# Kernel optimization log

Hardware: AMD Instinct MI355X
Metric: run time of the kernel (lower is better)

## Reference

```python
import jax, jax.numpy as jnp
import numpy as np

NELEMS = 1_000_000
FEAT = 128
NSEG = 1024


def setup_inputs() -> dict:
    key = jax.random.key(0)
    k1, k2 = jax.random.split(key)
    memory = jax.random.normal(k1, (NELEMS, FEAT), dtype=jnp.float32)
    m_batch = jnp.sort(jax.random.randint(k2, (NELEMS,), 0, NSEG, dtype=jnp.int64))
    return {"memory": memory, "m_batch": m_batch, "num_segments": NSEG}


def reference(memory, m_batch, num_segments):
    # torch.sparse.sum over dim=1 of a [nbatches, nelems, F] COO tensor built from
    # (batch, arange) indices == per-batch segment sum of memory rows.
    return jax.ops.segment_sum(memory, m_batch, num_segments=num_segments)
```

## Files before the change

kernel.cpp:

```cpp
#include <hip/hip_runtime.h>


#define FEAT 128
#define F4 (FEAT / 4)
#define ROWLANES 16
#define THREADS (F4 * ROWLANES)

typedef float f32x4 __attribute__((ext_vector_type(4)));

__global__ __launch_bounds__(THREADS, 8) void segsum_fused(
        const f32x4* __restrict__ mem,
        const int* __restrict__ seg,
        f32x4* __restrict__ out,
        int nelems) {
    const int b    = blockIdx.x;
    const int lane = threadIdx.x & (F4 - 1);
    const int rl   = threadIdx.x >> 5;

    __shared__ int sb[2];

    if (threadIdx.x < 64) {
        const int half = threadIdx.x >> 5;
        const int j    = threadIdx.x & 31;
        const int t    = b + half;

        int lo = 0, len = nelems;
        #pragma unroll
        for (int round = 0; round < 4; ++round) {
            int pos = lo + (int)(((long long)j * len) >> 5);
            int v = seg[pos];
            unsigned long long m = __ballot(v < t);
            unsigned mh = half ? (unsigned)(m >> 32) : (unsigned)(m & 0xffffffffull);
            int c = __popc(mh);
            int pcm1 = lo + (int)(((long long)(c - 1) * len) >> 5);
            int pc   = (c < 32) ? (lo + (int)(((long long)c * len) >> 5)) : (lo + len);
            int newlo = (c > 0) ? pcm1 : lo;
            int newhi = (c > 0) ? pc : lo;
            lo = newlo;
            len = newhi - newlo;
        }
        int v = (j < len) ? seg[lo + j] : 0x7fffffff;
        unsigned long long m = __ballot(v < t);
        unsigned mh = half ? (unsigned)(m >> 32) : (unsigned)(m & 0xffffffffull);
        if (j == 0) sb[half] = lo + __popc(mh);
    }
    __syncthreads();

    const int start = sb[0];
    const int end   = sb[1];

    f32x4 a0 = (f32x4)0.f, a1 = (f32x4)0.f, a2 = (f32x4)0.f, a3 = (f32x4)0.f;

    int r = start + rl;
    for (; r + 3 * ROWLANES < end; r += 4 * ROWLANES) {
        f32x4 v0 = __builtin_nontemporal_load(&mem[(size_t)r * F4 + lane]);
        f32x4 v1 = __builtin_nontemporal_load(&mem[(size_t)(r + ROWLANES) * F4 + lane]);
        f32x4 v2 = __builtin_nontemporal_load(&mem[(size_t)(r + 2 * ROWLANES) * F4 + lane]);
        f32x4 v3 = __builtin_nontemporal_load(&mem[(size_t)(r + 3 * ROWLANES) * F4 + lane]);
        a0 += v0; a1 += v1; a2 += v2; a3 += v3;
    }
    for (; r < end; r += ROWLANES) {
        a0 += __builtin_nontemporal_load(&mem[(size_t)r * F4 + lane]);
    }
    a0 += a1; a2 += a3; a0 += a2;

    __shared__ f32x4 red[ROWLANES][F4];
    red[rl][lane] = a0;
    __syncthreads();
    if (rl < 4) {
        red[rl][lane] = red[rl][lane] + red[rl + 4][lane] +
                        red[rl + 8][lane] + red[rl + 12][lane];
    }
    __syncthreads();
    if (rl == 0) {
        f32x4 s = red[0][lane] + red[1][lane] + red[2][lane] + red[3][lane];
        out[(size_t)b * F4 + lane] = s;
    }
}

extern "C" void kernel_launch(void* const* d_in, const int* in_sizes, int n_in,
                              void* d_out, int out_size, void* d_ws, size_t ws_size,
                              hipStream_t stream) {
    const f32x4* mem = (const f32x4*)d_in[0];
    const int* seg = (const int*)d_in[1];
    f32x4* out = (f32x4*)d_out;

    const int nelems = in_sizes[1];
    const int nseg = out_size / FEAT;

    segsum_fused<<<nseg, THREADS, 0, stream>>>(mem, seg, out, nelems);
}
```

Measured before the change: 81.57 us.

## Split each segment across four blocks and combine with atomic adds

Each segment is now handled by four smaller blocks (256 threads instead of 512), each summing a quarter of the segment's rows, so the grid has more, lighter blocks to spread across CUs. The partial sums are combined with float atomicAdd into an output that is zeroed first by a memset. The cost is an extra memset launch, four times as many binary searches, atomic traffic, and a summation order that is no longer deterministic.

```diff
diff --git a/kernel.cpp b/kernel.cpp
--- a/kernel.cpp
+++ b/kernel.cpp
@@ -3,17 +3,20 @@
 
 #define FEAT 128
 #define F4 (FEAT / 4)
-#define ROWLANES 16
+#define ROWLANES 8
 #define THREADS (F4 * ROWLANES)
+#define SPLIT 4
 
 typedef float f32x4 __attribute__((ext_vector_type(4)));
 
-__global__ __launch_bounds__(THREADS, 8) void segsum_fused(
+__global__ __launch_bounds__(THREADS, 8) void segsum_split(
         const f32x4* __restrict__ mem,
         const int* __restrict__ seg,
-        f32x4* __restrict__ out,
+        float* __restrict__ out,
         int nelems) {
-    const int b    = blockIdx.x;
+    const int bid  = blockIdx.x;
+    const int s    = bid >> 2;
+    const int q    = bid & (SPLIT - 1);
     const int lane = threadIdx.x & (F4 - 1);
     const int rl   = threadIdx.x >> 5;
 
@@ -22,7 +25,7 @@
     if (threadIdx.x < 64) {
         const int half = threadIdx.x >> 5;
         const int j    = threadIdx.x & 31;
-        const int t    = b + half;
+        const int t    = s + half;
 
         int lo = 0, len = nelems;
         #pragma unroll
@@ -47,19 +50,21 @@
     __syncthreads();
 
     const int start = sb[0];
-    const int end   = sb[1];
+    const int len   = sb[1] - start;
+    const int r0    = start + (int)(((long long)q * len) / SPLIT);
+    const int r1    = start + (int)(((long long)(q + 1) * len) / SPLIT);
 
     f32x4 a0 = (f32x4)0.f, a1 = (f32x4)0.f, a2 = (f32x4)0.f, a3 = (f32x4)0.f;
 
-    int r = start + rl;
-    for (; r + 3 * ROWLANES < end; r += 4 * ROWLANES) {
+    int r = r0 + rl;
+    for (; r + 3 * ROWLANES < r1; r += 4 * ROWLANES) {
         f32x4 v0 = __builtin_nontemporal_load(&mem[(size_t)r * F4 + lane]);
         f32x4 v1 = __builtin_nontemporal_load(&mem[(size_t)(r + ROWLANES) * F4 + lane]);
         f32x4 v2 = __builtin_nontemporal_load(&mem[(size_t)(r + 2 * ROWLANES) * F4 + lane]);
         f32x4 v3 = __builtin_nontemporal_load(&mem[(size_t)(r + 3 * ROWLANES) * F4 + lane]);
         a0 += v0; a1 += v1; a2 += v2; a3 += v3;
     }
-    for (; r < end; r += ROWLANES) {
+    for (; r < r1; r += ROWLANES) {
         a0 += __builtin_nontemporal_load(&mem[(size_t)r * F4 + lane]);
     }
     a0 += a1; a2 += a3; a0 += a2;
@@ -67,14 +72,18 @@
     __shared__ f32x4 red[ROWLANES][F4];
     red[rl][lane] = a0;
     __syncthreads();
-    if (rl < 4) {
-        red[rl][lane] = red[rl][lane] + red[rl + 4][lane] +
-                        red[rl + 8][lane] + red[rl + 12][lane];
+    if (rl < 2) {
+        red[rl][lane] = red[rl][lane] + red[rl + 2][lane] +
+                        red[rl + 4][lane] + red[rl + 6][lane];
     }
     __syncthreads();
     if (rl == 0) {
-        f32x4 s = red[0][lane] + red[1][lane] + red[2][lane] + red[3][lane];
-        out[(size_t)b * F4 + lane] = s;
+        f32x4 v = red[0][lane] + red[1][lane];
+        float* o = out + (size_t)s * FEAT + lane * 4;
+        atomicAdd(o + 0, v.x);
+        atomicAdd(o + 1, v.y);
+        atomicAdd(o + 2, v.z);
+        atomicAdd(o + 3, v.w);
     }
 }
 
@@ -83,10 +92,12 @@
                               hipStream_t stream) {
     const f32x4* mem = (const f32x4*)d_in[0];
     const int* seg = (const int*)d_in[1];
-    f32x4* out = (f32x4*)d_out;
+    float* out = (float*)d_out;
 
     const int nelems = in_sizes[1];
     const int nseg = out_size / FEAT;
 
-    segsum_fused<<<nseg, THREADS, 0, stream>>>(mem, seg, out, nelems);
+    hipMemsetAsync(out, 0, (size_t)out_size * sizeof(float), stream);
+
+    segsum_split<<<nseg * SPLIT, THREADS, 0, stream>>>(mem, seg, out, nelems);
 }
```

After: 93.41 us. 14.5% more time.
